# Kernel tuning notes

Hardware: AMD Instinct MI355X
Metric: run time of the kernel (lower is better)

Reference implementation:

```python
import jax, jax.numpy as jnp
import numpy as np

B, H, N, M = 8192, 512, 1024, 128
EPS_COS = 1e-8   # torch cosine_similarity default eps
EPS_NORM = 1e-16 # normalization eps in forward


def _linear_params(key, fan_in, fan_out):
    # torch nn.Linear default init: U(-1/sqrt(fan_in), 1/sqrt(fan_in))
    lim = 1.0 / np.sqrt(fan_in)
    kw, kb = jax.random.split(key)
    W = jax.random.uniform(kw, (fan_out, fan_in), minval=-lim, maxval=lim, dtype=jnp.float32)
    b = jax.random.uniform(kb, (fan_out,), minval=-lim, maxval=lim, dtype=jnp.float32)
    return W, b


def setup_inputs() -> dict:
    key = jax.random.key(0)
    ks = jax.random.split(key, 8)
    Wk, bk = _linear_params(ks[0], H, M)
    Wb, bb = _linear_params(ks[1], H, 1)
    Wg, bg = _linear_params(ks[2], H, 1)
    Ws, bs = _linear_params(ks[3], H, N)
    Wgam, bgam = _linear_params(ks[4], H, 1)
    x = jax.random.normal(ks[5], (B, H), dtype=jnp.float32)
    # previous_state is an attention-weight vector over memory rows (sums to 1)
    previous_state = jax.nn.softmax(jax.random.normal(ks[6], (B, N), dtype=jnp.float32), axis=-1)
    memory = jax.random.normal(ks[7], (N, M), dtype=jnp.float32)
    return dict(x=x, previous_state=previous_state, memory=memory,
                Wk=Wk, bk=bk, Wb=Wb, bb=bb, Wg=Wg, bg=bg,
                Ws=Ws, bs=bs, Wgam=Wgam, bgam=bgam)


def _circular_convolution(w, s):
    # Full circular convolution over the memory axis:
    #   out[b, i] = sum_j w[b, j] * s[b, (i - j) mod N]
    # Implemented via FFT to avoid materializing a [B, N, N] shift matrix.
    out = jnp.fft.irfft(jnp.fft.rfft(w, axis=-1) * jnp.fft.rfft(s, axis=-1),
                        n=w.shape[-1], axis=-1)
    # conv of nonnegative weights is nonnegative; clamp tiny FFT round-off
    # negatives so the fractional power below stays well defined.
    return jnp.maximum(out, 0.0)


def reference(x, previous_state, memory, Wk, bk, Wb, bb, Wg, bg, Ws, bs, Wgam, bgam):
    k = x @ Wk.T + bk                                   # [B, M]
    beta = jax.nn.softplus(x @ Wb.T + bb)               # [B, 1]
    g = jax.nn.sigmoid(x @ Wg.T + bg)                   # [B, 1]
    s = jax.nn.softmax(x @ Ws.T + bs, axis=-1)          # [B, N]
    gamma = 1.0 + jax.nn.softplus(x @ Wgam.T + bgam)    # [B, 1]

    # cosine similarity between each key and each memory row -> [B, N]
    k_n = k / jnp.maximum(jnp.linalg.norm(k, axis=-1, keepdims=True), EPS_COS)
    m_n = memory / jnp.maximum(jnp.linalg.norm(memory, axis=-1, keepdims=True), EPS_COS)
    cos = k_n @ m_n.T                                   # [B, N]

    w_c = jax.nn.softmax(beta * cos, axis=1)            # content addressing
    w_g = g * w_c + (1.0 - g) * previous_state          # interpolation gate
    w_t = _circular_convolution(w_g, s)                 # location shift
    w = w_t ** gamma                                    # sharpening
    w = w / (jnp.sum(w, axis=1, keepdims=True) + EPS_NORM)

    read = w @ memory                                   # [B, M]
    return read, w
```

## Files before the change

kernel.cpp:

```cpp
#include <hip/hip_runtime.h>
#include <hip/hip_bf16.h>
#include <hip/hip_fp16.h>

typedef __attribute__((ext_vector_type(8))) short short8;
typedef __attribute__((ext_vector_type(4))) short short4v;
typedef __attribute__((ext_vector_type(4))) float f32x4;

#define B_ROWS 8192
#define HDIM 512
#define NDIM 1024
#define MDIM 128

__device__ __forceinline__ float softplusf(float z) {
  return fmaxf(z, 0.f) + log1pf(__expf(-fabsf(z)));
}
__device__ __forceinline__ unsigned short f2bfu(float f) {
  __hip_bfloat16 h = __float2bfloat16(f);
  return *reinterpret_cast<unsigned short*>(&h);
}
__device__ __forceinline__ short8 pack8(float4 a, float4 b) {
  short8 r;
  r[0] = (short)f2bfu(a.x); r[1] = (short)f2bfu(a.y);
  r[2] = (short)f2bfu(a.z); r[3] = (short)f2bfu(a.w);
  r[4] = (short)f2bfu(b.x); r[5] = (short)f2bfu(b.y);
// ... 43 lines not shown
    float zb = x0.x*b0.x + x0.y*b0.y + x0.z*b0.z + x0.w*b0.w
             + x1.x*b1.x + x1.y*b1.y + x1.z*b1.z + x1.w*b1.w;
    float zg = x0.x*g0.x + x0.y*g0.y + x0.z*g0.z + x0.w*g0.w
             + x1.x*g1.x + x1.y*g1.y + x1.z*g1.z + x1.w*g1.w;
    float zm = x0.x*m0.x + x0.y*m0.y + x0.z*m0.z + x0.w*m0.w
             + x1.x*m1.x + x1.y*m1.y + x1.z*m1.z + x1.w*m1.w;
#pragma unroll
    for (int o = 32; o; o >>= 1) {
      zb += __shfl_xor(zb, o); zg += __shfl_xor(zg, o); zm += __shfl_xor(zm, o);
    }
    if (lane == 0) {
      zb += bb[0]; zg += bg[0]; zm += bgam[0];
      bgg[b * 4 + 0] = softplusf(zb);
      bgg[b * 4 + 1] = 1.f / (1.f + __expf(-zg));
      bgg[b * 4 + 2] = 1.f + softplusf(zm);
    }
  } else {
    const int NS4 = NDIM * HDIM / 4;
    const int NK4 = MDIM * HDIM / 4;
    const int stride = 144 * 256;
    for (int i = (blk - 2560) * 256 + t; i < NS4 + NK4; i += stride) {
      const float* src; short* dst; int j = i;
      if (j < NS4) { src = Ws; dst = wsb; }
      else { j -= NS4; src = Wk; dst = wkb; }
      const float4 v = ((const float4*)src)[j];
      short4v o;
      o[0] = (short)f2bfu(v.x); o[1] = (short)f2bfu(v.y);
      o[2] = (short)f2bfu(v.z); o[3] = (short)f2bfu(v.w);
      ((short4v*)dst)[j] = o;
    }
  }
}

__global__ __launch_bounds__(256) void kgemm_cos(
    const short* __restrict__ xb, const short* __restrict__ wkb,
    const float* __restrict__ bk, const short* __restrict__ mn_bf,
    __half* __restrict__ cosbH)
{
  __shared__ __align__(16) short sA[32][40];
  __shared__ __align__(16) short sW[128][40];
  __shared__ __align__(16) short skhat[32][136];
  __shared__ __align__(16) short sMN[128][136];
  __shared__ float snorm[4][32];
  __shared__ float sinv[32];

  const int tid = threadIdx.x, lane = tid & 63, wid = tid >> 6;
  const int bm = blockIdx.x;
  const int fr = lane & 15, kg = (lane >> 4) << 3;
  const int rbase = (lane >> 4) << 2;

  f32x4 acc[2][2] = {};
  for (int k0 = 0; k0 < HDIM; k0 += 32) {
    if (k0) __syncthreads();
    if (tid < 128) {
      const int row = tid >> 2, c0 = (tid & 3) * 8;
      *(short8*)(&sA[row][c0]) =
          *(const short8*)(xb + (size_t)(bm * 32 + row) * HDIM + k0 + c0);
    }
#pragma unroll
    for (int u = tid; u < 512; u += 256) {
      const int row = u >> 2, c0 = (u & 3) * 8;
      *(short8*)(&sW[row][c0]) =
          *(const short8*)(wkb + (size_t)row * HDIM + k0 + c0);
    }
    __syncthreads();

    short8 af[2], bf[2];
#pragma unroll
    for (int i = 0; i < 2; i++) af[i] = *(const short8*)(&sA[i * 16 + fr][kg]);
#pragma unroll
    for (int n = 0; n < 2; n++) bf[n] = *(const short8*)(&sW[wid * 32 + n * 16 + fr][kg]);
#pragma unroll
    for (int i = 0; i < 2; i++)
#pragma unroll
      for (int n = 0; n < 2; n++)
        acc[i][n] = __builtin_amdgcn_mfma_f32_16x16x32_bf16(af[i], bf[n], acc[i][n], 0, 0, 0);
  }

  float z[2][2][4];
#pragma unroll
  for (int i = 0; i < 2; i++)
#pragma unroll
    for (int n = 0; n < 2; n++) {
      const float bv = bk[wid * 32 + n * 16 + fr];
#pragma unroll
      for (int r = 0; r < 4; r++) z[i][n][r] = acc[i][n][r] + bv;
    }
#pragma unroll
  for (int i = 0; i < 2; i++)
#pragma unroll
    for (int r = 0; r < 4; r++) {
      float sq = z[i][0][r] * z[i][0][r] + z[i][1][r] * z[i][1][r];
      sq += __shfl_xor(sq, 1); sq += __shfl_xor(sq, 2);
      sq += __shfl_xor(sq, 4); sq += __shfl_xor(sq, 8);
      if (fr == 0) snorm[wid][i * 16 + rbase + r] = sq;
    }
  __syncthreads();
  if (tid < 32) {
    const float nn = snorm[0][tid] + snorm[1][tid] + snorm[2][tid] + snorm[3][tid];
    sinv[tid] = 1.f / fmaxf(sqrtf(nn), 1e-8f);
  }
  __syncthreads();
#pragma unroll
  for (int i = 0; i < 2; i++)
#pragma unroll
    for (int n = 0; n < 2; n++)
#pragma unroll
      for (int r = 0; r < 4; r++) {
        const int row = i * 16 + rbase + r;
        skhat[row][wid * 32 + n * 16 + fr] = (short)f2bfu(z[i][n][r] * sinv[row]);
      }

  for (int cc = 0; cc < 8; cc++) {
#pragma unroll
    for (int i = 0; i < 8; i++) {
      const int u = tid + i * 256;
      const int r = u >> 4, c0 = (u & 15) * 8;
      *(short8*)(&sMN[r][c0]) =
          *(const short8*)(mn_bf + (size_t)(cc * 128 + r) * MDIM + c0);
    }
    __syncthreads();

    f32x4 acc2[2][2] = {};
#pragma unroll
    for (int k0 = 0; k0 < 128; k0 += 32) {
      short8 af2[2], bf2[2];
#pragma unroll
      for (int i = 0; i < 2; i++)
        af2[i] = *(const short8*)(&skhat[i * 16 + fr][k0 + kg]);
#pragma unroll
      for (int n = 0; n < 2; n++)
        bf2[n] = *(const short8*)(&sMN[wid * 32 + n * 16 + fr][k0 + kg]);
#pragma unroll
      for (int i = 0; i < 2; i++)
#pragma unroll
        for (int n = 0; n < 2; n++)
          acc2[i][n] = __builtin_amdgcn_mfma_f32_16x16x32_bf16(af2[i], bf2[n], acc2[i][n], 0, 0, 0);
    }
    __syncthreads();

#pragma unroll
    for (int i = 0; i < 2; i++)
#pragma unroll
      for (int n = 0; n < 2; n++)
#pragma unroll
        for (int r = 0; r < 4; r++) {
          const int row = i * 16 + rbase + r;
          const int gc = cc * 128 + wid * 32 + n * 16 + fr;
          cosbH[(size_t)(bm * 32 + row) * NDIM + gc] = __float2half(acc2[i][n][r]);
        }
  }
}

template<int OUTMODE>
__global__ __launch_bounds__(256) void kgemm128(
    const short* __restrict__ A, const short* __restrict__ W,
    const float* __restrict__ bias, void* __restrict__ C,
    int ncols, int Kld, int ksplit, size_t cstride)
{
  __shared__ __align__(16) short sA[128 * 32];
  __shared__ __align__(16) short sB[128 * 32];

  const int tid = threadIdx.x, lane = tid & 63, wid = tid >> 6;
  const int bm = blockIdx.y, bn = blockIdx.x;
  const int wr = wid >> 1, wc = wid & 1;
  const int fr = lane & 15, kg = (lane >> 4) << 3;
  const int kbeg = blockIdx.z * ksplit, kend = kbeg + ksplit;

  f32x4 acc[4][4] = {};

  for (int k0 = kbeg; k0 < kend; k0 += 32) {
    if (k0 != kbeg) __syncthreads();
#pragma unroll
    for (int j = 0; j < 2; j++) {
      const int c = tid + j * 256;
      const short* g = A + (size_t)(bm * 128 + (c >> 2)) * Kld + k0 + (c & 3) * 8;
      short* l = &sA[(j * 256 + wid * 64) * 8];
      __builtin_amdgcn_global_load_lds(
          (const __attribute__((address_space(1))) void*)g,
          (__attribute__((address_space(3))) void*)l, 16, 0, 0);
    }
#pragma unroll
    for (int j = 0; j < 2; j++) {
      const int c = tid + j * 256;
      const short* g = W + (size_t)(bn * 128 + (c >> 2)) * Kld + k0 + (c & 3) * 8;
      short* l = &sB[(j * 256 + wid * 64) * 8];
      __builtin_amdgcn_global_load_lds(
          (const __attribute__((address_space(1))) void*)g,
          (__attribute__((address_space(3))) void*)l, 16, 0, 0);
    }
    __syncthreads();

    short8 af[4], bf[4];
#pragma unroll
    for (int m = 0; m < 4; m++)
      af[m] = *(const short8*)(&sA[(wr * 64 + m * 16 + fr) * 32 + kg]);
#pragma unroll
    for (int n = 0; n < 4; n++)
      bf[n] = *(const short8*)(&sB[(wc * 64 + n * 16 + fr) * 32 + kg]);

#pragma unroll
    for (int m = 0; m < 4; m++)
#pragma unroll
      for (int n = 0; n < 4; n++)
        acc[m][n] = __builtin_amdgcn_mfma_f32_16x16x32_bf16(af[m], bf[n], acc[m][n], 0, 0, 0);
  }

#pragma unroll
  for (int m = 0; m < 4; m++)
#pragma unroll
    for (int n = 0; n < 4; n++) {
      const int gr = bm * 128 + wr * 64 + m * 16 + ((lane >> 4) << 2);
      const int gc = bn * 128 + wc * 64 + n * 16 + fr;
      const float bv = bias ? bias[gc] : 0.f;
#pragma unroll
      for (int r = 0; r < 4; r++) {
        const float v = acc[m][n][r] + bv;
        const size_t idx = (size_t)(gr + r) * ncols + gc + blockIdx.z * cstride;
        if constexpr (OUTMODE == 0) ((float*)C)[idx] = v;
        else ((__half*)C)[idx] = __float2half(v);
      }
    }
}

__global__ __launch_bounds__(256) void reduce4(const float* __restrict__ p,
                                               float* __restrict__ out)
{
  const int i = blockIdx.x * 256 + threadIdx.x;
  const float4* p4 = (const float4*)p;
  const float4 a = p4[i], b = p4[i + 262144], c = p4[i + 524288], d = p4[i + 786432];
  ((float4*)out)[i] = make_float4(a.x + b.x + c.x + d.x, a.y + b.y + c.y + d.y,
                                  a.z + b.z + c.z + d.z, a.w + b.w + c.w + d.w);
}

#define ANG0 (-0.0061359231515425650f)

template<int ST>
__device__ __forceinline__ void fft_mid(const float* __restrict__ sr,
                                        const float* __restrict__ si,
                                        float* __restrict__ dr,
                                        float* __restrict__ di, int tid,
                                        int j0, int j1, int j2, int j3)
{
  const int ls = 2 * ST, s = 1 << ls;
  const int p = tid >> ls, q = tid & (s - 1), tb = tid & ~(s - 1);
  const float a0r = sr[j0], a0i = si[j0], a1r = sr[j1], a1i = si[j1];
  const float a2r = sr[j2], a2i = si[j2], a3r = sr[j3], a3i = si[j3];
  const float b0r = a0r + a2r, b0i = a0i + a2i, b1r = a1r + a3r, b1i = a1i + a3i;
  const float b2r = a0r - a2r, b2i = a0i - a2i, b3r = a1r - a3r, b3i = a1i - a3i;
  const float A0r = b0r + b1r, A0i = b0i + b1i;
  const float A1r = b2r + b3i, A1i = b2i - b3r;
  const float A2r = b0r - b1r, A2i = b0i - b1i;
  const float A3r = b2r - b3i, A3i = b2i + b3r;
  const int o = q + 4 * s * p;
  dr[pad(o)] = A0r; di[pad(o)] = A0i;
  if constexpr (ST < 4) {
    float s1, c1; __sincosf(ANG0 * (float)tb, &s1, &c1);
    const float c2 = c1 * c1 - s1 * s1, s2 = 2.f * s1 * c1;
    const float c3 = c1 * c2 - s1 * s2, s3 = s1 * c2 + c1 * s2;
    dr[pad(o + s)]     = A1r * c1 - A1i * s1; di[pad(o + s)]     = A1r * s1 + A1i * c1;
    dr[pad(o + 2 * s)] = A2r * c2 - A2i * s2; di[pad(o + 2 * s)] = A2r * s2 + A2i * c2;
    dr[pad(o + 3 * s)] = A3r * c3 - A3i * s3; di[pad(o + 3 * s)] = A3r * s3 + A3i * c3;
  } else {
    dr[pad(o + s)]     = A1r; di[pad(o + s)]     = A1i;
    dr[pad(o + 2 * s)] = A2r; di[pad(o + 2 * s)] = A2i;
    dr[pad(o + 3 * s)] = A3r; di[pad(o + 3 * s)] = A3i;
  }
  __syncthreads();
}

template<int J>
__device__ __forceinline__ void fft512_mid(const float* __restrict__ sr,
                                           const float* __restrict__ si,
                                           float* __restrict__ dr,
                                           float* __restrict__ di, int tid)
{
  if (tid < 128) {
    constexpr int s  = (J == 1) ? 2 : (J == 2) ? 8 : 32;
    constexpr int ns = (J == 1) ? 256 : (J == 2) ? 64 : 16;
    constexpr int ls = (J == 1) ? 1 : (J == 2) ? 3 : 5;
    const int p = tid >> ls, q = tid & (s - 1);
    const float a0r = sr[pad(tid)],       a0i = si[pad(tid)];
    const float a1r = sr[pad(tid + 128)], a1i = si[pad(tid + 128)];
    const float a2r = sr[pad(tid + 256)], a2i = si[pad(tid + 256)];
    const float a3r = sr[pad(tid + 384)], a3i = si[pad(tid + 384)];
    const float b0r = a0r + a2r, b0i = a0i + a2i, b1r = a1r + a3r, b1i = a1i + a3i;
    const float b2r = a0r - a2r, b2i = a0i - a2i, b3r = a1r - a3r, b3i = a1i - a3i;
    const float A0r = b0r + b1r, A0i = b0i + b1i;
    const float A1r = b2r + b3i, A1i = b2i - b3r;
    const float A2r = b0r - b1r, A2i = b0i - b1i;
    const float A3r = b2r - b3i, A3i = b2i + b3r;
    float s1, c1; __sincosf((-6.283185307179586f / (float)ns) * (float)p, &s1, &c1);
    const float c2 = c1 * c1 - s1 * s1, s2 = 2.f * s1 * c1;
    const float c3 = c1 * c2 - s1 * s2, s3 = s1 * c2 + c1 * s2;
    const int o = q + 4 * s * p;
    dr[pad(o)]         = A0r;                 di[pad(o)]         = A0i;
    dr[pad(o + s)]     = A1r * c1 - A1i * s1; di[pad(o + s)]     = A1r * s1 + A1i * c1;
    dr[pad(o + 2 * s)] = A2r * c2 - A2i * s2; di[pad(o + 2 * s)] = A2r * s2 + A2i * c2;
    dr[pad(o + 3 * s)] = A3r * c3 - A3i * s3; di[pad(o + 3 * s)] = A3r * s3 + A3i * c3;
  }
  __syncthreads();
}

__global__ __launch_bounds__(256) void rowpass(
    const __half* __restrict__ slogH, const __half* __restrict__ cosbH,
    const float* __restrict__ bgg, const float* __restrict__ prev,
    float* __restrict__ wout, short* __restrict__ wbf)
{
  __shared__ float bAr[1088], bAi[1088], bBr[1088], bBi[1088];
  __shared__ float sred[8];
  const int b = blockIdx.x, tid = threadIdx.x;
  const int lane = tid & 63, wid = tid >> 6;
  const int j0 = pad(tid), j1 = pad(tid + 256), j2 = pad(tid + 512), j3 = pad(tid + 768);

  const float beta = bgg[b * 4 + 0], g = bgg[b * 4 + 1], gamma = bgg[b * 4 + 2];

  float sv[4], cv[4];
  float e1 = 0.f, e2 = 0.f;
#pragma unroll
  for (int i = 0; i < 4; i++) {
    sv[i] = __expf(__half2float(slogH[(size_t)b * NDIM + tid + i * 256]));
    cv[i] = __expf(beta * __half2float(cosbH[(size_t)b * NDIM + tid + i * 256]));
    e1 += sv[i]; e2 += cv[i];
  }
#pragma unroll
  for (int o = 32; o; o >>= 1) { e1 += __shfl_xor(e1, o); e2 += __shfl_xor(e2, o); }
  if (lane == 0) { sred[wid * 2] = e1; sred[wid * 2 + 1] = e2; }
  __syncthreads();
  const float r1 = 1.f / (sred[0] + sred[2] + sred[4] + sred[6]);
  const float r2 = 1.f / (sred[1] + sred[3] + sred[5] + sred[7]);

  float s1, c1; __sincosf(ANG0 * (float)tid, &s1, &c1);
  const float c2 = c1 * c1 - s1 * s1, s2 = 2.f * s1 * c1;
  const float c3 = c1 * c2 - s1 * s2, s3 = s1 * c2 + c1 * s2;

  {
    float ar[4], ai[4];
#pragma unroll
    for (int i = 0; i < 4; i++) {
      const int idx = tid + i * 256;
      const float pv = prev[(size_t)b * NDIM + idx];
      ar[i] = g * cv[i] * r2 + (1.f - g) * pv;
      ai[i] = sv[i] * r1;
    }
    const float b0r = ar[0] + ar[2], b0i = ai[0] + ai[2];
    const float b1r = ar[1] + ar[3], b1i = ai[1] + ai[3];
    const float b2r = ar[0] - ar[2], b2i = ai[0] - ai[2];
    const float b3r = ar[1] - ar[3], b3i = ai[1] - ai[3];
    const float A0r = b0r + b1r, A0i = b0i + b1i;
    const float A1r = b2r + b3i, A1i = b2i - b3r;
    const float A2r = b0r - b1r, A2i = b0i - b1i;
    const float A3r = b2r - b3i, A3i = b2i + b3r;
    const int o4 = 4 * tid;
    bBr[pad(o4)]     = A0r;                  bBi[pad(o4)]     = A0i;
    bBr[pad(o4 + 1)] = A1r * c1 - A1i * s1;  bBi[pad(o4 + 1)] = A1r * s1 + A1i * c1;
    bBr[pad(o4 + 2)] = A2r * c2 - A2i * s2;  bBi[pad(o4 + 2)] = A2r * s2 + A2i * c2;
    bBr[pad(o4 + 3)] = A3r * c3 - A3i * s3;  bBi[pad(o4 + 3)] = A3r * s3 + A3i * c3;
  }
  __syncthreads();

  fft_mid<1>(bBr, bBi, bAr, bAi, tid, j0, j1, j2, j3);
  fft_mid<2>(bAr, bAi, bBr, bBi, tid, j0, j1, j2, j3);
  fft_mid<3>(bBr, bBi, bAr, bAi, tid, j0, j1, j2, j3);
  fft_mid<4>(bAr, bAi, bBr, bBi, tid, j0, j1, j2, j3);

#pragma unroll
  for (int i = 0; i < 2; i++) {
    const int k = tid + i * 256;
    const int kp = pad(k), rp = pad((1024 - k) & 1023);
    const float Zkr = bBr[kp], Zki = bBi[kp];
    const float Zrr = bBr[rp], Zri = bBi[rp];
    const float Wr = 0.5f * (Zkr + Zrr), Wi = 0.5f * (Zki - Zri);
    const float Sr = 0.5f * (Zki + Zri), Si = 0.5f * (Zrr - Zkr);
    bAr[kp] = Wr * Sr - Wi * Si;
    bAi[kp] = Wr * Si + Wi * Sr;
  }
  if (tid == 0) {
    const int kp = pad(512);
    bAr[kp] = bBr[kp] * bBi[kp];
    bAi[kp] = 0.f;
  }
  __syncthreads();

  {
    float es, ec; __sincosf(0.0061359231515425650f * (float)tid, &es, &ec);
    const float P0r = bAr[pad(tid)],        P0i = bAi[pad(tid)];
    const float Pa0r = bAr[pad(512 - tid)], Pa0i = bAi[pad(512 - tid)];
    const float S0r = P0r + Pa0r, S0i = P0i - Pa0i;
    const float D0r = P0r - Pa0r, D0i = P0i + Pa0i;
    const float Q0r = S0r - es * D0r - ec * D0i;
    const float Q0i = S0i + ec * D0r - es * D0i;
    const float P1r = bAr[pad(tid + 256)],  P1i = bAi[pad(tid + 256)];
    const float Pa1r = bAr[pad(256 - tid)], Pa1i = bAi[pad(256 - tid)];
    const float S1r = P1r + Pa1r, S1i = P1i - Pa1i;
    const float D1r = P1r - Pa1r, D1i = P1i + Pa1i;
    const float Q1r = S1r - ec * D1r + es * D1i;
    const float Q1i = S1i - es * D1r - ec * D1i;
    const float ur = Q0r, ui = -Q0i, vr = Q1r, vi = -Q1i;
    float ts, tc; __sincosf(-0.012271846303085130f * (float)tid, &ts, &tc);
    const float d_r = ur - vr, d_i = ui - vi;
    bBr[pad(2 * tid)]     = ur + vr;             bBi[pad(2 * tid)]     = ui + vi;
    bBr[pad(2 * tid + 1)] = d_r * tc - d_i * ts; bBi[pad(2 * tid + 1)] = d_r * ts + d_i * tc;
  }
  __syncthreads();

  fft512_mid<1>(bBr, bBi, bAr, bAi, tid);
  fft512_mid<2>(bAr, bAi, bBr, bBi, tid);
  fft512_mid<3>(bBr, bBi, bAr, bAi, tid);

  if (tid < 128) {
    const int i0 = pad(tid), i1 = pad(tid + 128), i2 = pad(tid + 256), i3 = pad(tid + 384);
    const float a0r = bAr[i0], a0i = bAi[i0], a1r = bAr[i1], a1i = bAi[i1];
    const float a2r = bAr[i2], a2i = bAi[i2], a3r = bAr[i3], a3i = bAi[i3];
    const float b0r = a0r + a2r, b0i = a0i + a2i, b1r = a1r + a3r, b1i = a1i + a3i;
    const float b2r = a0r - a2r, b2i = a0i - a2i, b3r = a1r - a3r, b3i = a1i - a3i;
    bBr[i0] = b0r + b1r; bBi[i0] = b0i + b1i;
    bBr[i1] = b2r + b3i; bBi[i1] = b2i - b3r;
    bBr[i2] = b0r - b1r; bBi[i2] = b0i - b1i;
    bBr[i3] = b2r - b3i; bBi[i3] = b2i + b3r;
  }
  __syncthreads();

  const int m0 = pad(2 * tid), m1 = pad(2 * tid + 1);
  float xv[4];
  xv[0] =  bBr[m0] * (1.f / 1024.f);
  xv[1] = -bBi[m0] * (1.f / 1024.f);
  xv[2] =  bBr[m1] * (1.f / 1024.f);
  xv[3] = -bBi[m1] * (1.f / 1024.f);

  float wt[4]; float esum = 0.f;
#pragma unroll
  for (int i = 0; i < 4; i++) {
    const float v = fmaxf(xv[i], 0.f);
    const float p = (v > 0.f) ? __expf(gamma * __logf(v)) : 0.f;
    wt[i] = p; esum += p;
  }
#pragma unroll
  for (int o = 32; o; o >>= 1) esum += __shfl_xor(esum, o);
  if (lane == 0) sred[wid] = esum;
  __syncthreads();
  const float rn = 1.f / (sred[0] + sred[1] + sred[2] + sred[3] + 1e-16f);
  const float w0 = wt[0] * rn, w1 = wt[1] * rn, w2 = wt[2] * rn, w3 = wt[3] * rn;
  *(float4*)(wout + (size_t)b * NDIM + 4 * tid) = make_float4(w0, w1, w2, w3);
  short4v wb;
  wb[0] = (short)f2bfu(w0); wb[1] = (short)f2bfu(w1);
  wb[2] = (short)f2bfu(w2); wb[3] = (short)f2bfu(w3);
  *(short4v*)(wbf + (size_t)b * NDIM + 4 * tid) = wb;
}

extern "C" void kernel_launch(void* const* d_in, const int* in_sizes, int n_in,
                              void* d_out, int out_size, void* d_ws, size_t ws_size,
                              hipStream_t stream)
{
  const float* x    = (const float*)d_in[0];
  const float* prev = (const float*)d_in[1];
  const float* mem  = (const float*)d_in[2];
  const float* Wk   = (const float*)d_in[3];
  const float* bk   = (const float*)d_in[4];
  const float* Wb   = (const float*)d_in[5];
  const float* bb   = (const float*)d_in[6];
  const float* Wg   = (const float*)d_in[7];
  const float* bg   = (const float*)d_in[8];
  const float* Ws   = (const float*)d_in[9];
  const float* bs   = (const float*)d_in[10];
  const float* Wgam = (const float*)d_in[11];
  const float* bgam = (const float*)d_in[12];

  char* ws = (char*)d_ws;
  short*  mn_bf   = (short*) (ws + 0);
  short*  memT_bf = (short*) (ws + 262144);
  float*  bgg     = (float*) (ws + 524288);
  __half* slogH   = (__half*)(ws + 655360);
  __half* cosbH   = (__half*)(ws + 17432576);
  short*  xb      = (short*) (ws + 34209792);
  short*  wsb     = (short*) (ws + 42598400);
  short*  wkb     = (short*) (ws + 43646976);
  short*  wbf     = (short*) (ws + 43778048);
  float*  rpart   = (float*) (ws + 60555264);

  float* readout = (float*)d_out;
  float* wout = readout + (size_t)B_ROWS * MDIM;

  prep_all<<<2704, 256, 0, stream>>>(x, Ws, Wk, mem, Wb, bb, Wg, bg, Wgam, bgam,
                                     xb, wsb, wkb, mn_bf, memT_bf, bgg);
  kgemm_cos<<<B_ROWS / 32, 256, 0, stream>>>(xb, wkb, bk, mn_bf, cosbH);
  kgemm128<1><<<dim3(NDIM / 128, B_ROWS / 128, 1), 256, 0, stream>>>(
      xb, wsb, bs, slogH, NDIM, HDIM, HDIM, 0);
  rowpass<<<B_ROWS, 256, 0, stream>>>(slogH, cosbH, bgg, prev, wout, wbf);
  kgemm128<0><<<dim3(1, B_ROWS / 128, 4), 256, 0, stream>>>(
      wbf, memT_bf, nullptr, rpart, MDIM, NDIM, 256, (size_t)B_ROWS * MDIM);
  reduce4<<<1024, 256, 0, stream>>>(rpart, readout);
}
```

Measured before the change: 117.9 us.

## Merge cosine and shift-logit GEMMs into one launch; process two rows per FFT block

The cosine-similarity GEMM and the shift-logit GEMM now run as a single heterogeneous kernel: the first 256 blocks compute cosines and the remaining 512 compute slog tiles, sharing one shared-memory buffer. This removes a launch and lets the two independent GEMMs run concurrently. The row-pass FFT kernel is rewritten to handle two batch rows per 256-thread block, so every thread is busy in the radix-4 stages where half the threads used to idle, and twiddle computation is shared across both rows. The cost is doubled shared memory per FFT block, which may lower occupancy, and heterogeneous blocks in the merged kernel may be imbalanced.

```diff
diff --git a/kernel.cpp b/kernel.cpp
--- a/kernel.cpp
+++ b/kernel.cpp
@@ -99,113 +99,80 @@
   }
 }
 
-__global__ __launch_bounds__(256) void kgemm_cos(
+__global__ __launch_bounds__(256) void heads(
     const short* __restrict__ xb, const short* __restrict__ wkb,
     const float* __restrict__ bk, const short* __restrict__ mn_bf,
-    __half* __restrict__ cosbH)
-{
-  __shared__ __align__(16) short sA[32][40];
-  __shared__ __align__(16) short sW[128][40];
-  __shared__ __align__(16) short skhat[32][136];
-  __shared__ __align__(16) short sMN[128][136];
-  __shared__ float snorm[4][32];
-  __shared__ float sinv[32];
-
+    __half* __restrict__ cosbH,
+    const short* __restrict__ wsb, const float* __restrict__ bs,
+    __half* __restrict__ slogH)
+{
+  __shared__ __align__(16) char smem[56960];
   const int tid = threadIdx.x, lane = tid & 63, wid = tid >> 6;
-  const int bm = blockIdx.x;
   const int fr = lane & 15, kg = (lane >> 4) << 3;
-  const int rbase = (lane >> 4) << 2;
-
-  f32x4 acc[2][2] = {};
-  for (int k0 = 0; k0 < HDIM; k0 += 32) {
-    if (k0) __syncthreads();
-    if (tid < 128) {
-      const int row = tid >> 2, c0 = (tid & 3) * 8;
-      *(short8*)(&sA[row][c0]) =
-          *(const short8*)(xb + (size_t)(bm * 32 + row) * HDIM + k0 + c0);
-    }
-#pragma unroll
-    for (int u = tid; u < 512; u += 256) {
-      const int row = u >> 2, c0 = (u & 3) * 8;
-      *(short8*)(&sW[row][c0]) =
-          *(const short8*)(wkb + (size_t)row * HDIM + k0 + c0);
-    }
+
+  if (blockIdx.x < 256) {
+    short (*sA)[40]     = (short(*)[40])(smem);
+    short (*sW)[40]     = (short(*)[40])(smem + 2560);
+    short (*skhat)[136] = (short(*)[136])(smem + 12800);
+    short (*sMN)[136]   = (short(*)[136])(smem + 21504);
+    float (*snorm)[32]  = (float(*)[32])(smem + 56320);
+    float* sinv         = (float*)(smem + 56832);
+
+    const int bm = blockIdx.x;
+    const int rbase = (lane >> 4) << 2;
+
+    f32x4 acc[2][2] = {};
+    for (int k0 = 0; k0 < HDIM; k0 += 32) {
+      if (k0) __syncthreads();
+      if (tid < 128) {
+        const int row = tid >> 2, c0 = (tid & 3) * 8;
+        *(short8*)(&sA[row][c0]) =
+            *(const short8*)(xb + (size_t)(bm * 32 + row) * HDIM + k0 + c0);
+      }
+#pragma unroll
+      for (int u = tid; u < 512; u += 256) {
+        const int row = u >> 2, c0 = (u & 3) * 8;
+        *(short8*)(&sW[row][c0]) =
+            *(const short8*)(wkb + (size_t)row * HDIM + k0 + c0);
+      }
+      __syncthreads();
+
+      short8 af[2], bf[2];
+#pragma unroll
+      for (int i = 0; i < 2; i++) af[i] = *(const short8*)(&sA[i * 16 + fr][kg]);
+#pragma unroll
+      for (int n = 0; n < 2; n++) bf[n] = *(const short8*)(&sW[wid * 32 + n * 16 + fr][kg]);
+#pragma unroll
+      for (int i = 0; i < 2; i++)
+#pragma unroll
+        for (int n = 0; n < 2; n++)
+          acc[i][n] = __builtin_amdgcn_mfma_f32_16x16x32_bf16(af[i], bf[n], acc[i][n], 0, 0, 0);
+    }
+
+    float z[2][2][4];
+#pragma unroll
+    for (int i = 0; i < 2; i++)
+#pragma unroll
+      for (int n = 0; n < 2; n++) {
+        const float bv = bk[wid * 32 + n * 16 + fr];
+#pragma unroll
+        for (int r = 0; r < 4; r++) z[i][n][r] = acc[i][n][r] + bv;
+      }
+#pragma unroll
+    for (int i = 0; i < 2; i++)
+#pragma unroll
+      for (int r = 0; r < 4; r++) {
+        float sq = z[i][0][r] * z[i][0][r] + z[i][1][r] * z[i][1][r];
+        sq += __shfl_xor(sq, 1); sq += __shfl_xor(sq, 2);
+        sq += __shfl_xor(sq, 4); sq += __shfl_xor(sq, 8);
+        if (fr == 0) snorm[wid][i * 16 + rbase + r] = sq;
+      }
     __syncthreads();
-
-    short8 af[2], bf[2];
-#pragma unroll
-    for (int i = 0; i < 2; i++) af[i] = *(const short8*)(&sA[i * 16 + fr][kg]);
-#pragma unroll
-    for (int n = 0; n < 2; n++) bf[n] = *(const short8*)(&sW[wid * 32 + n * 16 + fr][kg]);
-#pragma unroll
-    for (int i = 0; i < 2; i++)
-#pragma unroll
-      for (int n = 0; n < 2; n++)
-        acc[i][n] = __builtin_amdgcn_mfma_f32_16x16x32_bf16(af[i], bf[n], acc[i][n], 0, 0, 0);
-  }
-
-  float z[2][2][4];
-#pragma unroll
-  for (int i = 0; i < 2; i++)
-#pragma unroll
-    for (int n = 0; n < 2; n++) {
-      const float bv = bk[wid * 32 + n * 16 + fr];
-#pragma unroll
-      for (int r = 0; r < 4; r++) z[i][n][r] = acc[i][n][r] + bv;
-    }
-#pragma unroll
-  for (int i = 0; i < 2; i++)
-#pragma unroll
-    for (int r = 0; r < 4; r++) {
-      float sq = z[i][0][r] * z[i][0][r] + z[i][1][r] * z[i][1][r];
-      sq += __shfl_xor(sq, 1); sq += __shfl_xor(sq, 2);
-      sq += __shfl_xor(sq, 4); sq += __shfl_xor(sq, 8);
-      if (fr == 0) snorm[wid][i * 16 + rbase + r] = sq;
-    }
-  __syncthreads();
-  if (tid < 32) {
-    const float nn = snorm[0][tid] + snorm[1][tid] + snorm[2][tid] + snorm[3][tid];
-    sinv[tid] = 1.f / fmaxf(sqrtf(nn), 1e-8f);
-  }
-  __syncthreads();
-#pragma unroll
-  for (int i = 0; i < 2; i++)
-#pragma unroll
-    for (int n = 0; n < 2; n++)
-#pragma unroll
-      for (int r = 0; r < 4; r++) {
-        const int row = i * 16 + rbase + r;
-        skhat[row][wid * 32 + n * 16 + fr] = (short)f2bfu(z[i][n][r] * sinv[row]);
-      }
-
-  for (int cc = 0; cc < 8; cc++) {
-#pragma unroll
-    for (int i = 0; i < 8; i++) {
-      const int u = tid + i * 256;
-      const int r = u >> 4, c0 = (u & 15) * 8;
-      *(short8*)(&sMN[r][c0]) =
-          *(const short8*)(mn_bf + (size_t)(cc * 128 + r) * MDIM + c0);
+    if (tid < 32) {
+      const float nn = snorm[0][tid] + snorm[1][tid] + snorm[2][tid] + snorm[3][tid];
+      sinv[tid] = 1.f / fmaxf(sqrtf(nn), 1e-8f);
     }
     __syncthreads();
-
-    f32x4 acc2[2][2] = {};
-#pragma unroll
-    for (int k0 = 0; k0 < 128; k0 += 32) {
-      short8 af2[2], bf2[2];
-#pragma unroll
-      for (int i = 0; i < 2; i++)
-        af2[i] = *(const short8*)(&skhat[i * 16 + fr][k0 + kg]);
-#pragma unroll
-      for (int n = 0; n < 2; n++)
-        bf2[n] = *(const short8*)(&sMN[wid * 32 + n * 16 + fr][k0 + kg]);
-#pragma unroll
-      for (int i = 0; i < 2; i++)
-#pragma unroll
-        for (int n = 0; n < 2; n++)
-          acc2[i][n] = __builtin_amdgcn_mfma_f32_16x16x32_bf16(af2[i], bf2[n], acc2[i][n], 0, 0, 0);
-    }
-    __syncthreads();
-
 #pragma unroll
     for (int i = 0; i < 2; i++)
 #pragma unroll
@@ -213,17 +180,109 @@
 #pragma unroll
         for (int r = 0; r < 4; r++) {
           const int row = i * 16 + rbase + r;
-          const int gc = cc * 128 + wid * 32 + n * 16 + fr;
-          cosbH[(size_t)(bm * 32 + row) * NDIM + gc] = __float2half(acc2[i][n][r]);
+          skhat[row][wid * 32 + n * 16 + fr] = (short)f2bfu(z[i][n][r] * sinv[row]);
         }
-  }
-}
-
-template<int OUTMODE>
-__global__ __launch_bounds__(256) void kgemm128(
+
+    for (int cc = 0; cc < 8; cc++) {
+#pragma unroll
+      for (int i = 0; i < 8; i++) {
+        const int u = tid + i * 256;
+        const int r = u >> 4, c0 = (u & 15) * 8;
+        *(short8*)(&sMN[r][c0]) =
+            *(const short8*)(mn_bf + (size_t)(cc * 128 + r) * MDIM + c0);
+      }
+      __syncthreads();
+
+      f32x4 acc2[2][2] = {};
+#pragma unroll
+      for (int k0 = 0; k0 < 128; k0 += 32) {
+        short8 af2[2], bf2[2];
+#pragma unroll
+        for (int i = 0; i < 2; i++)
+          af2[i] = *(const short8*)(&skhat[i * 16 + fr][k0 + kg]);
+#pragma unroll
+        for (int n = 0; n < 2; n++)
+          bf2[n] = *(const short8*)(&sMN[wid * 32 + n * 16 + fr][k0 + kg]);
+#pragma unroll
+        for (int i = 0; i < 2; i++)
+#pragma unroll
+          for (int n = 0; n < 2; n++)
+            acc2[i][n] = __builtin_amdgcn_mfma_f32_16x16x32_bf16(af2[i], bf2[n], acc2[i][n], 0, 0, 0);
+      }
+      __syncthreads();
+
+#pragma unroll
+      for (int i = 0; i < 2; i++)
+#pragma unroll
+        for (int n = 0; n < 2; n++)
+#pragma unroll
+          for (int r = 0; r < 4; r++) {
+            const int row = i * 16 + rbase + r;
+            const int gc = cc * 128 + wid * 32 + n * 16 + fr;
+            cosbH[(size_t)(bm * 32 + row) * NDIM + gc] = __float2half(acc2[i][n][r]);
+          }
+    }
+  } else {
+    short* sA = (short*)smem;
+    short* sB = (short*)(smem + 8192);
+    const int blk2 = blockIdx.x - 256;
+    const int bm = blk2 >> 3, bn = blk2 & 7;
+    const int wr = wid >> 1, wc = wid & 1;
+
+    f32x4 acc[4][4] = {};
+    for (int k0 = 0; k0 < HDIM; k0 += 32) {
+      if (k0) __syncthreads();
+#pragma unroll
+      for (int j = 0; j < 2; j++) {
+        const int c = tid + j * 256;
+        const short* g = xb + (size_t)(bm * 128 + (c >> 2)) * HDIM + k0 + (c & 3) * 8;
+        short* l = sA + (j * 256 + wid * 64) * 8;
+        __builtin_amdgcn_global_load_lds(
+            (const __attribute__((address_space(1))) void*)g,
+            (__attribute__((address_space(3))) void*)l, 16, 0, 0);
+      }
+#pragma unroll
+      for (int j = 0; j < 2; j++) {
+        const int c = tid + j * 256;
+        const short* g = wsb + (size_t)(bn * 128 + (c >> 2)) * HDIM + k0 + (c & 3) * 8;
+        short* l = sB + (j * 256 + wid * 64) * 8;
+        __builtin_amdgcn_global_load_lds(
+            (const __attribute__((address_space(1))) void*)g,
+            (__attribute__((address_space(3))) void*)l, 16, 0, 0);
+      }
+      __syncthreads();
+
+      short8 af[4], bf[4];
+#pragma unroll
+      for (int m = 0; m < 4; m++)
+        af[m] = *(const short8*)(&sA[(wr * 64 + m * 16 + fr) * 32 + kg]);
+#pragma unroll
+      for (int n = 0; n < 4; n++)
+        bf[n] = *(const short8*)(&sB[(wc * 64 + n * 16 + fr) * 32 + kg]);
+#pragma unroll
+      for (int m = 0; m < 4; m++)
+#pragma unroll
+        for (int n = 0; n < 4; n++)
+          acc[m][n] = __builtin_amdgcn_mfma_f32_16x16x32_bf16(af[m], bf[n], acc[m][n], 0, 0, 0);
+    }
+
+#pragma unroll
+    for (int m = 0; m < 4; m++)
+#pragma unroll
+      for (int n = 0; n < 4; n++) {
+        const int gr = bm * 128 + wr * 64 + m * 16 + ((lane >> 4) << 2);
+        const int gc = bn * 128 + wc * 64 + n * 16 + fr;
+        const float bv = bs[gc];
+#pragma unroll
+        for (int r = 0; r < 4; r++)
+          slogH[(size_t)(gr + r) * NDIM + gc] = __float2half(acc[m][n][r] + bv);
+      }
+  }
+}
+
+__global__ __launch_bounds__(256) void kgemm_read(
     const short* __restrict__ A, const short* __restrict__ W,
-    const float* __restrict__ bias, void* __restrict__ C,
-    int ncols, int Kld, int ksplit, size_t cstride)
+    float* __restrict__ C, int ncols, int Kld, int ksplit, size_t cstride)
 {
   __shared__ __align__(16) short sA[128 * 32];
   __shared__ __align__(16) short sB[128 * 32];
@@ -279,14 +338,9 @@
     for (int n = 0; n < 4; n++) {
       const int gr = bm * 128 + wr * 64 + m * 16 + ((lane >> 4) << 2);
       const int gc = bn * 128 + wc * 64 + n * 16 + fr;
-      const float bv = bias ? bias[gc] : 0.f;
-#pragma unroll
-      for (int r = 0; r < 4; r++) {
-        const float v = acc[m][n][r] + bv;
-        const size_t idx = (size_t)(gr + r) * ncols + gc + blockIdx.z * cstride;
-        if constexpr (OUTMODE == 0) ((float*)C)[idx] = v;
-        else ((__half*)C)[idx] = __float2half(v);
-      }
+#pragma unroll
+      for (int r = 0; r < 4; r++)
+        C[(size_t)(gr + r) * ncols + gc + blockIdx.z * cstride] = acc[m][n][r];
     }
 }
 
@@ -303,112 +357,131 @@
 #define ANG0 (-0.0061359231515425650f)
 
 template<int ST>
-__device__ __forceinline__ void fft_mid(const float* __restrict__ sr,
-                                        const float* __restrict__ si,
-                                        float* __restrict__ dr,
-                                        float* __restrict__ di, int tid,
-                                        int j0, int j1, int j2, int j3)
+__device__ __forceinline__ void fft_mid2(const float (*sr)[1088], const float (*si)[1088],
+                                         float (*dr)[1088], float (*di)[1088], int tid,
+                                         int j0, int j1, int j2, int j3)
 {
   const int ls = 2 * ST, s = 1 << ls;
   const int p = tid >> ls, q = tid & (s - 1), tb = tid & ~(s - 1);
-  const float a0r = sr[j0], a0i = si[j0], a1r = sr[j1], a1i = si[j1];
-  const float a2r = sr[j2], a2i = si[j2], a3r = sr[j3], a3i = si[j3];
+  const int o = q + 4 * s * p;
+  float c1 = 1.f, s1 = 0.f, c2 = 1.f, s2 = 0.f, c3 = 1.f, s3 = 0.f;
+  if constexpr (ST < 4) {
+    __sincosf(ANG0 * (float)tb, &s1, &c1);
+    c2 = c1 * c1 - s1 * s1; s2 = 2.f * s1 * c1;
+    c3 = c1 * c2 - s1 * s2; s3 = s1 * c2 + c1 * s2;
+  }
+#pragma unroll
+  for (int r = 0; r < 2; r++) {
+    const float a0r = sr[r][j0], a0i = si[r][j0], a1r = sr[r][j1], a1i = si[r][j1];
+    const float a2r = sr[r][j2], a2i = si[r][j2], a3r = sr[r][j3], a3i = si[r][j3];
+    const float b0r = a0r + a2r, b0i = a0i + a2i, b1r = a1r + a3r, b1i = a1i + a3i;
+    const float b2r = a0r - a2r, b2i = a0i - a2i, b3r = a1r - a3r, b3i = a1i - a3i;
+    const float A0r = b0r + b1r, A0i = b0i + b1i;
+    const float A1r = b2r + b3i, A1i = b2i - b3r;
+    const float A2r = b0r - b1r, A2i = b0i - b1i;
+    const float A3r = b2r - b3i, A3i = b2i + b3r;
+    dr[r][pad(o)] = A0r; di[r][pad(o)] = A0i;
+    if constexpr (ST < 4) {
+      dr[r][pad(o + s)]     = A1r * c1 - A1i * s1; di[r][pad(o + s)]     = A1r * s1 + A1i * c1;
+      dr[r][pad(o + 2 * s)] = A2r * c2 - A2i * s2; di[r][pad(o + 2 * s)] = A2r * s2 + A2i * c2;
+      dr[r][pad(o + 3 * s)] = A3r * c3 - A3i * s3; di[r][pad(o + 3 * s)] = A3r * s3 + A3i * c3;
+    } else {
+      dr[r][pad(o + s)]     = A1r; di[r][pad(o + s)]     = A1i;
+      dr[r][pad(o + 2 * s)] = A2r; di[r][pad(o + 2 * s)] = A2i;
+      dr[r][pad(o + 3 * s)] = A3r; di[r][pad(o + 3 * s)] = A3i;
+    }
+  }
+  __syncthreads();
+}
+
+template<int J>
+__device__ __forceinline__ void fft512_mid2(const float (*sr)[1088], const float (*si)[1088],
+                                            float (*dr)[1088], float (*di)[1088], int tid)
+{
+  constexpr int s  = (J == 1) ? 2 : (J == 2) ? 8 : 32;
+  constexpr int ns = (J == 1) ? 256 : (J == 2) ? 64 : 16;
+  constexpr int ls = (J == 1) ? 1 : (J == 2) ? 3 : 5;
+  const int rw = tid >> 7, t = tid & 127;
+  const int p = t >> ls, q = t & (s - 1);
+  const float a0r = sr[rw][pad(t)],       a0i = si[rw][pad(t)];
+  const float a1r = sr[rw][pad(t + 128)], a1i = si[rw][pad(t + 128)];
+  const float a2r = sr[rw][pad(t + 256)], a2i = si[rw][pad(t + 256)];
+  const float a3r = sr[rw][pad(t + 384)], a3i = si[rw][pad(t + 384)];
   const float b0r = a0r + a2r, b0i = a0i + a2i, b1r = a1r + a3r, b1i = a1i + a3i;
   const float b2r = a0r - a2r, b2i = a0i - a2i, b3r = a1r - a3r, b3i = a1i - a3i;
   const float A0r = b0r + b1r, A0i = b0i + b1i;
   const float A1r = b2r + b3i, A1i = b2i - b3r;
   const float A2r = b0r - b1r, A2i = b0i - b1i;
   const float A3r = b2r - b3i, A3i = b2i + b3r;
+  float s1, c1; __sincosf((-6.283185307179586f / (float)ns) * (float)p, &s1, &c1);
+  const float c2 = c1 * c1 - s1 * s1, s2 = 2.f * s1 * c1;
+  const float c3 = c1 * c2 - s1 * s2, s3 = s1 * c2 + c1 * s2;
   const int o = q + 4 * s * p;
-  dr[pad(o)] = A0r; di[pad(o)] = A0i;
-  if constexpr (ST < 4) {
-    float s1, c1; __sincosf(ANG0 * (float)tb, &s1, &c1);
-    const float c2 = c1 * c1 - s1 * s1, s2 = 2.f * s1 * c1;
-    const float c3 = c1 * c2 - s1 * s2, s3 = s1 * c2 + c1 * s2;
-    dr[pad(o + s)]     = A1r * c1 - A1i * s1; di[pad(o + s)]     = A1r * s1 + A1i * c1;
-    dr[pad(o + 2 * s)] = A2r * c2 - A2i * s2; di[pad(o + 2 * s)] = A2r * s2 + A2i * c2;
-    dr[pad(o + 3 * s)] = A3r * c3 - A3i * s3; di[pad(o + 3 * s)] = A3r * s3 + A3i * c3;
-  } else {
-    dr[pad(o + s)]     = A1r; di[pad(o + s)]     = A1i;
-    dr[pad(o + 2 * s)] = A2r; di[pad(o + 2 * s)] = A2i;
-    dr[pad(o + 3 * s)] = A3r; di[pad(o + 3 * s)] = A3i;
-  }
-  __syncthreads();
-}
-
-template<int J>
-__device__ __forceinline__ void fft512_mid(const float* __restrict__ sr,
-                                           const float* __restrict__ si,
-                                           float* __restrict__ dr,
-                                           float* __restrict__ di, int tid)
-{
-  if (tid < 128) {
-    constexpr int s  = (J == 1) ? 2 : (J == 2) ? 8 : 32;
-    constexpr int ns = (J == 1) ? 256 : (J == 2) ? 64 : 16;
-    constexpr int ls = (J == 1) ? 1 : (J == 2) ? 3 : 5;
-    const int p = tid >> ls, q = tid & (s - 1);
-    const float a0r = sr[pad(tid)],       a0i = si[pad(tid)];
-    const float a1r = sr[pad(tid + 128)], a1i = si[pad(tid + 128)];
-    const float a2r = sr[pad(tid + 256)], a2i = si[pad(tid + 256)];
-    const float a3r = sr[pad(tid + 384)], a3i = si[pad(tid + 384)];
-    const float b0r = a0r + a2r, b0i = a0i + a2i, b1r = a1r + a3r, b1i = a1i + a3i;
-    const float b2r = a0r - a2r, b2i = a0i - a2i, b3r = a1r - a3r, b3i = a1i - a3i;
-    const float A0r = b0r + b1r, A0i = b0i + b1i;
-    const float A1r = b2r + b3i, A1i = b2i - b3r;
-    const float A2r = b0r - b1r, A2i = b0i - b1i;
-    const float A3r = b2r - b3i, A3i = b2i + b3r;
-    float s1, c1; __sincosf((-6.283185307179586f / (float)ns) * (float)p, &s1, &c1);
-    const float c2 = c1 * c1 - s1 * s1, s2 = 2.f * s1 * c1;
-    const float c3 = c1 * c2 - s1 * s2, s3 = s1 * c2 + c1 * s2;
-    const int o = q + 4 * s * p;
-    dr[pad(o)]         = A0r;                 di[pad(o)]         = A0i;
-    dr[pad(o + s)]     = A1r * c1 - A1i * s1; di[pad(o + s)]     = A1r * s1 + A1i * c1;
-    dr[pad(o + 2 * s)] = A2r * c2 - A2i * s2; di[pad(o + 2 * s)] = A2r * s2 + A2i * c2;
-    dr[pad(o + 3 * s)] = A3r * c3 - A3i * s3; di[pad(o + 3 * s)] = A3r * s3 + A3i * c3;
-  }
-  __syncthreads();
-}
-
-__global__ __launch_bounds__(256) void rowpass(
+  dr[rw][pad(o)]         = A0r;                 di[rw][pad(o)]         = A0i;
+  dr[rw][pad(o + s)]     = A1r * c1 - A1i * s1; di[rw][pad(o + s)]     = A1r * s1 + A1i * c1;
+  dr[rw][pad(o + 2 * s)] = A2r * c2 - A2i * s2; di[rw][pad(o + 2 * s)] = A2r * s2 + A2i * c2;
+  dr[rw][pad(o + 3 * s)] = A3r * c3 - A3i * s3; di[rw][pad(o + 3 * s)] = A3r * s3 + A3i * c3;
+  __syncthreads();
+}
+
+__global__ __launch_bounds__(256) void rowpass2(
     const __half* __restrict__ slogH, const __half* __restrict__ cosbH,
     const float* __restrict__ bgg, const float* __restrict__ prev,
     float* __restrict__ wout, short* __restrict__ wbf)
 {
-  __shared__ float bAr[1088], bAi[1088], bBr[1088], bBi[1088];
-  __shared__ float sred[8];
-  const int b = blockIdx.x, tid = threadIdx.x;
+  __shared__ float bAr[2][1088], bAi[2][1088], bBr[2][1088], bBi[2][1088];
+  __shared__ float sred[16];
+  const int bp = blockIdx.x, tid = threadIdx.x;
   const int lane = tid & 63, wid = tid >> 6;
   const int j0 = pad(tid), j1 = pad(tid + 256), j2 = pad(tid + 512), j3 = pad(tid + 768);
-
-  const float beta = bgg[b * 4 + 0], g = bgg[b * 4 + 1], gamma = bgg[b * 4 + 2];
-
-  float sv[4], cv[4];
-  float e1 = 0.f, e2 = 0.f;
-#pragma unroll
-  for (int i = 0; i < 4; i++) {
-    sv[i] = __expf(__half2float(slogH[(size_t)b * NDIM + tid + i * 256]));
-    cv[i] = __expf(beta * __half2float(cosbH[(size_t)b * NDIM + tid + i * 256]));
-    e1 += sv[i]; e2 += cv[i];
-  }
-#pragma unroll
-  for (int o = 32; o; o >>= 1) { e1 += __shfl_xor(e1, o); e2 += __shfl_xor(e2, o); }
-  if (lane == 0) { sred[wid * 2] = e1; sred[wid * 2 + 1] = e2; }
-  __syncthreads();
-  const float r1 = 1.f / (sred[0] + sred[2] + sred[4] + sred[6]);
-  const float r2 = 1.f / (sred[1] + sred[3] + sred[5] + sred[7]);
+  const int b0 = bp * 2;
+
+  float beta[2], g[2], gamma[2];
+#pragma unroll
+  for (int r = 0; r < 2; r++) {
+    beta[r]  = bgg[(b0 + r) * 4 + 0];
+    g[r]     = bgg[(b0 + r) * 4 + 1];
+    gamma[r] = bgg[(b0 + r) * 4 + 2];
+  }
+
+  float sv[2][4], cv[2][4], e1[2] = {0.f, 0.f}, e2[2] = {0.f, 0.f};
+#pragma unroll
+  for (int r = 0; r < 2; r++)
+#pragma unroll
+    for (int i = 0; i < 4; i++) {
+      sv[r][i] = __expf(__half2float(slogH[(size_t)(b0 + r) * NDIM + tid + i * 256]));
+      cv[r][i] = __expf(beta[r] * __half2float(cosbH[(size_t)(b0 + r) * NDIM + tid + i * 256]));
+      e1[r] += sv[r][i]; e2[r] += cv[r][i];
+    }
+#pragma unroll
+  for (int o = 32; o; o >>= 1) {
+    e1[0] += __shfl_xor(e1[0], o); e2[0] += __shfl_xor(e2[0], o);
+    e1[1] += __shfl_xor(e1[1], o); e2[1] += __shfl_xor(e2[1], o);
+  }
+  if (lane == 0) {
+    sred[wid * 4 + 0] = e1[0]; sred[wid * 4 + 1] = e2[0];
+    sred[wid * 4 + 2] = e1[1]; sred[wid * 4 + 3] = e2[1];
+  }
+  __syncthreads();
+  float r1[2], r2[2];
+  r1[0] = 1.f / (sred[0] + sred[4] + sred[8]  + sred[12]);
+  r2[0] = 1.f / (sred[1] + sred[5] + sred[9]  + sred[13]);
+  r1[1] = 1.f / (sred[2] + sred[6] + sred[10] + sred[14]);
+  r2[1] = 1.f / (sred[3] + sred[7] + sred[11] + sred[15]);
 
   float s1, c1; __sincosf(ANG0 * (float)tid, &s1, &c1);
   const float c2 = c1 * c1 - s1 * s1, s2 = 2.f * s1 * c1;
   const float c3 = c1 * c2 - s1 * s2, s3 = s1 * c2 + c1 * s2;
 
-  {
+#pragma unroll
+  for (int r = 0; r < 2; r++) {
     float ar[4], ai[4];
 #pragma unroll
     for (int i = 0; i < 4; i++) {
       const int idx = tid + i * 256;
-      const float pv = prev[(size_t)b * NDIM + idx];
-      ar[i] = g * cv[i] * r2 + (1.f - g) * pv;
-      ai[i] = sv[i] * r1;
+      const float pv = prev[(size_t)(b0 + r) * NDIM + idx];
+      ar[i] = g[r] * cv[r][i] * r2[r] + (1.f - g[r]) * pv;
+      ai[i] = sv[r][i] * r1[r];
     }
     const float b0r = ar[0] + ar[2], b0i = ai[0] + ai[2];
     const float b1r = ar[1] + ar[3], b1i = ai[1] + ai[3];
@@ -419,100 +492,117 @@
     const float A2r = b0r - b1r, A2i = b0i - b1i;
     const float A3r = b2r - b3i, A3i = b2i + b3r;
     const int o4 = 4 * tid;
-    bBr[pad(o4)]     = A0r;                  bBi[pad(o4)]     = A0i;
-    bBr[pad(o4 + 1)] = A1r * c1 - A1i * s1;  bBi[pad(o4 + 1)] = A1r * s1 + A1i * c1;
-    bBr[pad(o4 + 2)] = A2r * c2 - A2i * s2;  bBi[pad(o4 + 2)] = A2r * s2 + A2i * c2;
-    bBr[pad(o4 + 3)] = A3r * c3 - A3i * s3;  bBi[pad(o4 + 3)] = A3r * s3 + A3i * c3;
-  }
-  __syncthreads();
-
-  fft_mid<1>(bBr, bBi, bAr, bAi, tid, j0, j1, j2, j3);
-  fft_mid<2>(bAr, bAi, bBr, bBi, tid, j0, j1, j2, j3);
-  fft_mid<3>(bBr, bBi, bAr, bAi, tid, j0, j1, j2, j3);
-  fft_mid<4>(bAr, bAi, bBr, bBi, tid, j0, j1, j2, j3);
-
-#pragma unroll
-  for (int i = 0; i < 2; i++) {
-    const int k = tid + i * 256;
-    const int kp = pad(k), rp = pad((1024 - k) & 1023);
-    const float Zkr = bBr[kp], Zki = bBi[kp];
-    const float Zrr = bBr[rp], Zri = bBi[rp];
-    const float Wr = 0.5f * (Zkr + Zrr), Wi = 0.5f * (Zki - Zri);
-    const float Sr = 0.5f * (Zki + Zri), Si = 0.5f * (Zrr - Zkr);
-    bAr[kp] = Wr * Sr - Wi * Si;
-    bAi[kp] = Wr * Si + Wi * Sr;
-  }
-  if (tid == 0) {
+    bBr[r][pad(o4)]     = A0r;                  bBi[r][pad(o4)]     = A0i;
+    bBr[r][pad(o4 + 1)] = A1r * c1 - A1i * s1;  bBi[r][pad(o4 + 1)] = A1r * s1 + A1i * c1;
+    bBr[r][pad(o4 + 2)] = A2r * c2 - A2i * s2;  bBi[r][pad(o4 + 2)] = A2r * s2 + A2i * c2;
+    bBr[r][pad(o4 + 3)] = A3r * c3 - A3i * s3;  bBi[r][pad(o4 + 3)] = A3r * s3 + A3i * c3;
+  }
+  __syncthreads();
+
+  fft_mid2<1>(bBr, bBi, bAr, bAi, tid, j0, j1, j2, j3);
+  fft_mid2<2>(bAr, bAi, bBr, bBi, tid, j0, j1, j2, j3);
+  fft_mid2<3>(bBr, bBi, bAr, bAi, tid, j0, j1, j2, j3);
+  fft_mid2<4>(bAr, bAi, bBr, bBi, tid, j0, j1, j2, j3);
+
+#pragma unroll
+  for (int r = 0; r < 2; r++)
+#pragma unroll
+    for (int i = 0; i < 2; i++) {
+      const int k = tid + i * 256;
+      const int kp = pad(k), rp = pad((1024 - k) & 1023);
+      const float Zkr = bBr[r][kp], Zki = bBi[r][kp];
+      const float Zrr = bBr[r][rp], Zri = bBi[r][rp];
+      const float Wr = 0.5f * (Zkr + Zrr), Wi = 0.5f * (Zki - Zri);
+      const float Sr = 0.5f * (Zki + Zri), Si = 0.5f * (Zrr - Zkr);
+      bAr[r][kp] = Wr * Sr - Wi * Si;
+      bAi[r][kp] = Wr * Si + Wi * Sr;
+    }
+  if (tid < 2) {
     const int kp = pad(512);
-    bAr[kp] = bBr[kp] * bBi[kp];
-    bAi[kp] = 0.f;
+    bAr[tid][kp] = bBr[tid][kp] * bBi[tid][kp];
+    bAi[tid][kp] = 0.f;
   }
   __syncthreads();
 
   {
     float es, ec; __sincosf(0.0061359231515425650f * (float)tid, &es, &ec);
-    const float P0r = bAr[pad(tid)],        P0i = bAi[pad(tid)];
-    const float Pa0r = bAr[pad(512 - tid)], Pa0i = bAi[pad(512 - tid)];
-    const float S0r = P0r + Pa0r, S0i = P0i - Pa0i;
-    const float D0r = P0r - Pa0r, D0i = P0i + Pa0i;
-    const float Q0r = S0r - es * D0r - ec * D0i;
-    const float Q0i = S0i + ec * D0r - es * D0i;
-    const float P1r = bAr[pad(tid + 256)],  P1i = bAi[pad(tid + 256)];
-    const float Pa1r = bAr[pad(256 - tid)], Pa1i = bAi[pad(256 - tid)];
-    const float S1r = P1r + Pa1r, S1i = P1i - Pa1i;
-    const float D1r = P1r - Pa1r, D1i = P1i + Pa1i;
-    const float Q1r = S1r - ec * D1r + es * D1i;
-    const float Q1i = S1i - es * D1r - ec * D1i;
-    const float ur = Q0r, ui = -Q0i, vr = Q1r, vi = -Q1i;
     float ts, tc; __sincosf(-0.012271846303085130f * (float)tid, &ts, &tc);
-    const float d_r = ur - vr, d_i = ui - vi;
-    bBr[pad(2 * tid)]     = ur + vr;             bBi[pad(2 * tid)]     = ui + vi;
-    bBr[pad(2 * tid + 1)] = d_r * tc - d_i * ts; bBi[pad(2 * tid + 1)] = d_r * ts + d_i * tc;
-  }
-  __syncthreads();
-
-  fft512_mid<1>(bBr, bBi, bAr, bAi, tid);
-  fft512_mid<2>(bAr, bAi, bBr, bBi, tid);
-  fft512_mid<3>(bBr, bBi, bAr, bAi, tid);
-
-  if (tid < 128) {
-    const int i0 = pad(tid), i1 = pad(tid + 128), i2 = pad(tid + 256), i3 = pad(tid + 384);
-    const float a0r = bAr[i0], a0i = bAi[i0], a1r = bAr[i1], a1i = bAi[i1];
-    const float a2r = bAr[i2], a2i = bAi[i2], a3r = bAr[i3], a3i = bAi[i3];
+#pragma unroll
+    for (int r = 0; r < 2; r++) {
+      const float P0r = bAr[r][pad(tid)],        P0i = bAi[r][pad(tid)];
+      const float Pa0r = bAr[r][pad(512 - tid)], Pa0i = bAi[r][pad(512 - tid)];
+      const float S0r = P0r + Pa0r, S0i = P0i - Pa0i;
+      const float D0r = P0r - Pa0r, D0i = P0i + Pa0i;
+      const float Q0r = S0r - es * D0r - ec * D0i;
+      const float Q0i = S0i + ec * D0r - es * D0i;
+      const float P1r = bAr[r][pad(tid + 256)],  P1i = bAi[r][pad(tid + 256)];
+      const float Pa1r = bAr[r][pad(256 - tid)], Pa1i = bAi[r][pad(256 - tid)];
+      const float S1r = P1r + Pa1r, S1i = P1i - Pa1i;
+      const float D1r = P1r - Pa1r, D1i = P1i + Pa1i;
+      const float Q1r = S1r - ec * D1r + es * D1i;
+      const float Q1i = S1i - es * D1r - ec * D1i;
+      const float ur = Q0r, ui = -Q0i, vr = Q1r, vi = -Q1i;
+      const float d_r = ur - vr, d_i = ui - vi;
+      bBr[r][pad(2 * tid)]     = ur + vr;             bBi[r][pad(2 * tid)]     = ui + vi;
+      bBr[r][pad(2 * tid + 1)] = d_r * tc - d_i * ts; bBi[r][pad(2 * tid + 1)] = d_r * ts + d_i * tc;
+    }
+  }
+  __syncthreads();
+
+  fft512_mid2<1>(bBr, bBi, bAr, bAi, tid);
+  fft512_mid2<2>(bAr, bAi, bBr, bBi, tid);
+  fft512_mid2<3>(bBr, bBi, bAr, bAi, tid);
+
+  {
+    const int rw = tid >> 7, t = tid & 127;
+    const int i0 = pad(t), i1 = pad(t + 128), i2 = pad(t + 256), i3 = pad(t + 384);
+    const float a0r = bAr[rw][i0], a0i = bAi[rw][i0], a1r = bAr[rw][i1], a1i = bAi[rw][i1];
+    const float a2r = bAr[rw][i2], a2i = bAi[rw][i2], a3r = bAr[rw][i3], a3i = bAi[rw][i3];
     const float b0r = a0r + a2r, b0i = a0i + a2i, b1r = a1r + a3r, b1i = a1i + a3i;
     const float b2r = a0r - a2r, b2i = a0i - a2i, b3r = a1r - a3r, b3i = a1i - a3i;
-    bBr[i0] = b0r + b1r; bBi[i0] = b0i + b1i;
-    bBr[i1] = b2r + b3i; bBi[i1] = b2i - b3r;
-    bBr[i2] = b0r - b1r; bBi[i2] = b0i - b1i;
-    bBr[i3] = b2r - b3i; bBi[i3] = b2i + b3r;
+    bBr[rw][i0] = b0r + b1r; bBi[rw][i0] = b0i + b1i;
+    bBr[rw][i1] = b2r + b3i; bBi[rw][i1] = b2i - b3r;
+    bBr[rw][i2] = b0r - b1r; bBi[rw][i2] = b0i - b1i;
+    bBr[rw][i3] = b2r - b3i; bBi[rw][i3] = b2i + b3r;
   }
   __syncthreads();
 
   const int m0 = pad(2 * tid), m1 = pad(2 * tid + 1);
-  float xv[4];
-  xv[0] =  bBr[m0] * (1.f / 1024.f);
-  xv[1] = -bBi[m0] * (1.f / 1024.f);
-  xv[2] =  bBr[m1] * (1.f / 1024.f);
-  xv[3] = -bBi[m1] * (1.f / 1024.f);
-
-  float wt[4]; float esum = 0.f;
-#pragma unroll
-  for (int i = 0; i < 4; i++) {
-    const float v = fmaxf(xv[i], 0.f);
-    const float p = (v > 0.f) ? __expf(gamma * __logf(v)) : 0.f;
-    wt[i] = p; esum += p;
-  }
-#pragma unroll
-  for (int o = 32; o; o >>= 1) esum += __shfl_xor(esum, o);
-  if (lane == 0) sred[wid] = esum;
-  __syncthreads();
-  const float rn = 1.f / (sred[0] + sred[1] + sred[2] + sred[3] + 1e-16f);
-  const float w0 = wt[0] * rn, w1 = wt[1] * rn, w2 = wt[2] * rn, w3 = wt[3] * rn;
-  *(float4*)(wout + (size_t)b * NDIM + 4 * tid) = make_float4(w0, w1, w2, w3);
-  short4v wb;
-  wb[0] = (short)f2bfu(w0); wb[1] = (short)f2bfu(w1);
-  wb[2] = (short)f2bfu(w2); wb[3] = (short)f2bfu(w3);
-  *(short4v*)(wbf + (size_t)b * NDIM + 4 * tid) = wb;
+  float wt[2][4], esum[2] = {0.f, 0.f};
+#pragma unroll
+  for (int r = 0; r < 2; r++) {
+    float xv[4];
+    xv[0] =  bBr[r][m0] * (1.f / 1024.f);
+    xv[1] = -bBi[r][m0] * (1.f / 1024.f);
+    xv[2] =  bBr[r][m1] * (1.f / 1024.f);
+    xv[3] = -bBi[r][m1] * (1.f / 1024.f);
+#pragma unroll
+    for (int i = 0; i < 4; i++) {
+      const float v = fmaxf(xv[i], 0.f);
+      const float pq = (v > 0.f) ? __expf(gamma[r] * __logf(v)) : 0.f;
+      wt[r][i] = pq; esum[r] += pq;
+    }
+  }
+#pragma unroll
+  for (int o = 32; o; o >>= 1) {
+    esum[0] += __shfl_xor(esum[0], o);
+    esum[1] += __shfl_xor(esum[1], o);
+  }
+  if (lane == 0) { sred[wid * 2] = esum[0]; sred[wid * 2 + 1] = esum[1]; }
+  __syncthreads();
+  float rn[2];
+  rn[0] = 1.f / (sred[0] + sred[2] + sred[4] + sred[6] + 1e-16f);
+  rn[1] = 1.f / (sred[1] + sred[3] + sred[5] + sred[7] + 1e-16f);
+#pragma unroll
+  for (int r = 0; r < 2; r++) {
+    const float w0 = wt[r][0] * rn[r], w1 = wt[r][1] * rn[r];
+    const float w2 = wt[r][2] * rn[r], w3 = wt[r][3] * rn[r];
+    *(float4*)(wout + (size_t)(b0 + r) * NDIM + 4 * tid) = make_float4(w0, w1, w2, w3);
+    short4v wb;
+    wb[0] = (short)f2bfu(w0); wb[1] = (short)f2bfu(w1);
+    wb[2] = (short)f2bfu(w2); wb[3] = (short)f2bfu(w3);
+    *(short4v*)(wbf + (size_t)(b0 + r) * NDIM + 4 * tid) = wb;
+  }
 }
 
 extern "C" void kernel_launch(void* const* d_in, const int* in_sizes, int n_in,
@@ -550,11 +640,9 @@
 
   prep_all<<<2704, 256, 0, stream>>>(x, Ws, Wk, mem, Wb, bb, Wg, bg, Wgam, bgam,
                                      xb, wsb, wkb, mn_bf, memT_bf, bgg);
-  kgemm_cos<<<B_ROWS / 32, 256, 0, stream>>>(xb, wkb, bk, mn_bf, cosbH);
-  kgemm128<1><<<dim3(NDIM / 128, B_ROWS / 128, 1), 256, 0, stream>>>(
-      xb, wsb, bs, slogH, NDIM, HDIM, HDIM, 0);
-  rowpass<<<B_ROWS, 256, 0, stream>>>(slogH, cosbH, bgg, prev, wout, wbf);
-  kgemm128<0><<<dim3(1, B_ROWS / 128, 4), 256, 0, stream>>>(
-      wbf, memT_bf, nullptr, rpart, MDIM, NDIM, 256, (size_t)B_ROWS * MDIM);
+  heads<<<768, 256, 0, stream>>>(xb, wkb, bk, mn_bf, cosbH, wsb, bs, slogH);
+  rowpass2<<<B_ROWS / 2, 256, 0, stream>>>(slogH, cosbH, bgg, prev, wout, wbf);
+  kgemm_read<<<dim3(1, B_ROWS / 128, 4), 256, 0, stream>>>(
+      wbf, memT_bf, rpart, MDIM, NDIM, 256, (size_t)B_ROWS * MDIM);
   reduce4<<<1024, 256, 0, stream>>>(rpart, readout);
 }
```

Result: faster. 104.5 us (-11.4%).
